# Performance work log

Hardware: AMD Instinct MI355X
Metric: run time of the kernel (lower is better)

Reference implementation:

```python
import jax, jax.numpy as jnp
import numpy as np

D_MODEL = 1024
N_HEADS = 16
D_K = D_MODEL // N_HEADS


def setup_inputs() -> dict:
    key = jax.random.key(0)
    ks = jax.random.split(key, 11)
    B, S = 2, 2048
    scale = 1.0 / np.sqrt(D_MODEL)
    return {
        "query": jax.random.normal(ks[0], (B, S, D_MODEL), jnp.float32),
        "key": jax.random.normal(ks[1], (B, S, D_MODEL), jnp.float32),
        "value": jax.random.normal(ks[2], (B, S, D_MODEL), jnp.float32),
        "w_q": jax.random.normal(ks[3], (D_MODEL, D_MODEL), jnp.float32) * scale,
        "b_q": jnp.zeros((D_MODEL,), jnp.float32),
        "w_k": jax.random.normal(ks[4], (D_MODEL, D_MODEL), jnp.float32) * scale,
        "b_k": jnp.zeros((D_MODEL,), jnp.float32),
        "w_v": jax.random.normal(ks[5], (D_MODEL, D_MODEL), jnp.float32) * scale,
        "b_v": jnp.zeros((D_MODEL,), jnp.float32),
        "w_o": jax.random.normal(ks[6], (D_MODEL, D_MODEL), jnp.float32) * scale,
        "b_o": jnp.zeros((D_MODEL,), jnp.float32),
    }


def reference(query, key, value, w_q, b_q, w_k, b_k, w_v, b_v, w_o, b_o):
    B, S, _ = query.shape
    # Linear projections (torch Linear: x @ W.T + b), split heads -> (B, H, S, Dk)
    def proj(x, w, b):
        y = jnp.einsum('bsd,ed->bse', x, w) + b
        return y.reshape(B, -1, N_HEADS, D_K).transpose(0, 2, 1, 3)
    q = proj(query, w_q, b_q)
    k = proj(key, w_k, b_k)
    v = proj(value, w_v, b_v)
    # Scaled dot-product attention (full O(S^2) scores, faithful to source)
    scores = jnp.einsum('bhqd,bhkd->bhqk', q, k) / np.sqrt(D_K)
    attn = jax.nn.softmax(scores, axis=-1)
    out = jnp.einsum('bhqk,bhkd->bhqd', attn, v)  # (B, H, S, Dk)
    out = out.transpose(0, 2, 1, 3).reshape(B, S, D_MODEL)
    out = jnp.einsum('bsd,ed->bse', out, w_o) + b_o
    return out
```

## Files before the change

kernel.cpp:

```cpp
#include <hip/hip_runtime.h>
#include <hip/hip_bf16.h>

#define DM 1024
#define NH 16
#define DKH 64
#define BB 2
#define SS 2048
#define MM (BB*SS)

typedef __bf16 v8bf __attribute__((ext_vector_type(8)));
typedef float  v4f  __attribute__((ext_vector_type(4)));
typedef float  v16f __attribute__((ext_vector_type(16)));

__device__ __forceinline__ unsigned short f2bf(float f) {
    union { float f; unsigned int u; } v; v.f = f;
    unsigned int u = v.u;
    unsigned int r = (u + 0x7fffu + ((u >> 16) & 1u)) >> 16;
    return (unsigned short)r;
}

__device__ __forceinline__ int cvtpk(float lo, float hi) {
    int r;
    asm("v_cvt_pk_bf16_f32 %0, %1, %2" : "=v"(r) : "v"(lo), "v"(hi));
    return r;
}

__device__ __forceinline__ void pl32swap(int& a, int& b) {
    asm("v_permlane32_swap_b32 %0, %1" : "+v"(a), "+v"(b));
}

__device__ __forceinline__ void gl16(const unsigned short* g, unsigned short* l) {
    auto gp = reinterpret_cast<const __attribute__((address_space(1))) unsigned int*>(
        reinterpret_cast<uintptr_t>(g));
    auto lp = reinterpret_cast<__attribute__((address_space(3))) unsigned int*>(
        reinterpret_cast<uintptr_t>(l));
    __builtin_amdgcn_global_load_lds(gp, lp, 16, 0, 0);
}

__global__ __launch_bounds__(256) void cvt_to_bf16(
    const float* __restrict__ xq, const float* __restrict__ xk, const float* __restrict__ xv,
    const float* __restrict__ wq, const float* __restrict__ wk, const float* __restrict__ wv,
    const float* __restrict__ wo, unsigned short* __restrict__ dst)
{
    const int y = blockIdx.y;
    const float* src;
    size_t n, off;
    if (y < 3) {
        src = (y == 0) ? xq : (y == 1) ? xk : xv;
        n = (size_t)MM * DM;
        off = (size_t)y * MM * DM;
    } else {
        src = (y == 3) ? wq : (y == 4) ? wk : (y == 5) ? wv : wo;
        n = (size_t)DM * DM;
        off = (size_t)3 * MM * DM + (size_t)(y - 3) * DM * DM;
    }
    unsigned short* d = dst + off;
    const size_t stride = (size_t)gridDim.x * blockDim.x;
    for (size_t i = (size_t)blockIdx.x * blockDim.x + threadIdx.x; i * 8 < n; i += stride) {
        float4 a = ((const float4*)src)[2 * i];
        float4 b = ((const float4*)src)[2 * i + 1];
        uint4 o;
        o.x = (unsigned)cvtpk(a.x, a.y);
        o.y = (unsigned)cvtpk(a.z, a.w);
        o.z = (unsigned)cvtpk(b.x, b.y);
        o.w = (unsigned)cvtpk(b.z, b.w);
        ((uint4*)d)[i] = o;
    }
}

__global__ __launch_bounds__(256) void proj_qkv_b(
    const unsigned short* __restrict__ xb, const unsigned short* __restrict__ wb,
    const float* __restrict__ bq, const float* __restrict__ bk, const float* __restrict__ bv,
    unsigned short* __restrict__ q_ws, unsigned short* __restrict__ k_ws,
    unsigned short* __restrict__ vt_ws)
{
    const int z = blockIdx.z;
    const unsigned short* X = xb + (size_t)z * MM * DM;
    const unsigned short* W = wb + (size_t)z * DM * DM;
    const float* bias = (z == 0) ? bq : (z == 1) ? bk : bv;

    __shared__ unsigned short lA[2][128 * 32];
    __shared__ unsigned short lB[2][128 * 32];

    const int t = threadIdx.x;
    const int lane = t & 63, w = t >> 6;
    const int wm = w >> 1, wn = w & 1;
    const int g = lane >> 4, lr = lane & 15;

    const int orig = blockIdx.y * 8 + blockIdx.x;
    const int swz = (orig & 7) * 32 + (orig >> 3);
    const int mbase = (swz >> 3) * 128;
    const int nbase = (swz & 7) * 128;

    const int srow = lane >> 2;
    const int scol = (lane & 3) * 8;

    v4f acc[4][4];
#pragma unroll
    for (int i = 0; i < 4; ++i)
#pragma unroll
        for (int j = 0; j < 4; ++j)
            acc[i][j] = (v4f){0.f, 0.f, 0.f, 0.f};

    auto stage = [&](int bi, int kb) {
        gl16(X + (size_t)(mbase + w * 16 + srow) * DM + kb + scol,      &lA[bi][w * 512]);
        gl16(X + (size_t)(mbase + 64 + w * 16 + srow) * DM + kb + scol, &lA[bi][(w + 4) * 512]);
        gl16(W + (size_t)(nbase + w * 16 + srow) * DM + kb + scol,      &lB[bi][w * 512]);
        gl16(W + (size_t)(nbase + 64 + w * 16 + srow) * DM + kb + scol, &lB[bi][(w + 4) * 512]);
    };

    stage(0, 0);
    __syncthreads();
    int buf = 0;
    for (int ki = 0; ki < 32; ++ki) {
        if (ki + 1 < 32) stage(buf ^ 1, (ki + 1) * 32);

        v8bf af[4], bf4[4];
#pragma unroll
        for (int mt = 0; mt < 4; ++mt)
            af[mt] = *(const v8bf*)(&lA[buf][(wm * 64 + mt * 16 + lr) * 32 + g * 8]);
#pragma unroll
        for (int nt = 0; nt < 4; ++nt)
            bf4[nt] = *(const v8bf*)(&lB[buf][(wn * 64 + nt * 16 + lr) * 32 + g * 8]);
#pragma unroll
        for (int mt = 0; mt < 4; ++mt)
#pragma unroll
            for (int nt = 0; nt < 4; ++nt)
                acc[mt][nt] = __builtin_amdgcn_mfma_f32_16x16x32_bf16(af[mt], bf4[nt], acc[mt][nt], 0, 0, 0);

        __syncthreads();
        buf ^= 1;
    }

    const float scale = (z == 0) ? 0.18033688011112042f : 1.0f;
#pragma unroll
    for (int nt = 0; nt < 4; ++nt) {
        int e = nbase + wn * 64 + nt * 16 + lr;
        float bval = bias[e];
        int h = e >> 6, dk = e & 63;
#pragma unroll
        for (int mt = 0; mt < 4; ++mt) {
#pragma unroll
            for (int r = 0; r < 4; ++r) {
                int m = mbase + wm * 64 + mt * 16 + g * 4 + r;
                float val = (acc[mt][nt][r] + bval) * scale;
                unsigned short o = f2bf(val);
                int b = m >> 11, s = m & 2047;
                if (z == 2) {
                    vt_ws[((size_t)(b * NH + h) * DKH + dk) * SS + s] = o;
                } else {
                    unsigned short* dst = (z == 0) ? q_ws : k_ws;
                    dst[((size_t)(b * NH + h) * SS + s) * DKH + dk] = o;
                }
            }
        }
    }
}

#define KB 64
#define LDP 72
#define BUFS 4608

__global__ __launch_bounds__(256) void attn_kernel(
    const unsigned short* __restrict__ q_ws, const unsigned short* __restrict__ k_ws,
    const unsigned short* __restrict__ vt_ws, unsigned short* __restrict__ o_ws)
{
    __shared__ unsigned short lsBuf[2 * 2 * BUFS];

    const int t = threadIdx.x, l = t & 63, w = t >> 6;
    const int h = l >> 5, ql = l & 31;
    const int id = blockIdx.x;
    const int swzb = (id & 7) * 64 + (id >> 3);
    const int bh = swzb >> 4, qb = swzb & 15;
    const int q0 = qb * 128 + w * 32;

    const unsigned short* Kbase = k_ws + (size_t)bh * SS * DKH;
    const unsigned short* Vbase = vt_ws + (size_t)bh * DKH * SS;

    v8bf qf[4];
#pragma unroll
    for (int c = 0; c < 4; ++c)
        qf[c] = *(const v8bf*)(q_ws + ((size_t)bh * SS + q0 + ql) * DKH + c * 16 + h * 8);

    v16f oT[2];
#pragma unroll
    for (int d = 0; d < 2; ++d)
#pragma unroll
        for (int r = 0; r < 16; ++r) oT[d][r] = 0.f;
    float l_lane = 0.f;
    const v16f z16 = {};

    const int r0 = t >> 3, c0 = (t & 7) * 8;
    uint4 kst0, kst1, vst0, vst1;

    kst0 = *(const uint4*)(Kbase + (size_t)(r0)      * DKH + c0);
    kst1 = *(const uint4*)(Kbase + (size_t)(r0 + 32) * DKH + c0);
    vst0 = *(const uint4*)(Vbase + (size_t)(r0)      * SS + c0);
    vst1 = *(const uint4*)(Vbase + (size_t)(r0 + 32) * SS + c0);
    {
        unsigned short* Kp = lsBuf;
        unsigned short* Vp = lsBuf + BUFS;
        *(uint4*)&Kp[r0 * LDP + c0] = kst0;
        *(uint4*)&Kp[(r0 + 32) * LDP + c0] = kst1;
        *(uint4*)&Vp[r0 * LDP + c0] = vst0;
        *(uint4*)&Vp[(r0 + 32) * LDP + c0] = vst1;
    }
    kst0 = *(const uint4*)(Kbase + (size_t)(KB + r0)      * DKH + c0);
    kst1 = *(const uint4*)(Kbase + (size_t)(KB + r0 + 32) * DKH + c0);
    vst0 = *(const uint4*)(Vbase + (size_t)(r0)      * SS + KB + c0);
    vst1 = *(const uint4*)(Vbase + (size_t)(r0 + 32) * SS + KB + c0);
    __syncthreads();

    const int NT = SS / KB;
    int p = 0;
    for (int tt = 0; tt < NT; ++tt) {
        unsigned short* Kp = lsBuf + p * (2 * BUFS);
        unsigned short* Vp = Kp + BUFS;
        if (tt + 1 < NT) {
            unsigned short* Kn = lsBuf + (p ^ 1) * (2 * BUFS);
            unsigned short* Vn = Kn + BUFS;
            *(uint4*)&Kn[r0 * LDP + c0] = kst0;
            *(uint4*)&Kn[(r0 + 32) * LDP + c0] = kst1;
            *(uint4*)&Vn[r0 * LDP + c0] = vst0;
            *(uint4*)&Vn[(r0 + 32) * LDP + c0] = vst1;
        }
        if (tt + 2 < NT) {
            int kt2 = (tt + 2) * KB;
            kst0 = *(const uint4*)(Kbase + (size_t)(kt2 + r0)      * DKH + c0);
            kst1 = *(const uint4*)(Kbase + (size_t)(kt2 + r0 + 32) * DKH + c0);
            vst0 = *(const uint4*)(Vbase + (size_t)(r0)      * SS + kt2 + c0);
            vst1 = *(const uint4*)(Vbase + (size_t)(r0 + 32) * SS + kt2 + c0);
        }

        v16f sT[2];
        __builtin_amdgcn_s_setprio(1);
#pragma unroll
        for (int kb = 0; kb < 2; ++kb) {
            v8bf kf = *(const v8bf*)&Kp[(kb * 32 + ql) * LDP + h * 8];
            sT[kb] = __builtin_amdgcn_mfma_f32_32x32x16_bf16(kf, qf[0], z16, 0, 0, 0);
        }
#pragma unroll
        for (int c = 1; c < 4; ++c)
#pragma unroll
            for (int kb = 0; kb < 2; ++kb) {
                v8bf kf = *(const v8bf*)&Kp[(kb * 32 + ql) * LDP + c * 16 + h * 8];
                sT[kb] = __builtin_amdgcn_mfma_f32_32x32x16_bf16(kf, qf[c], sT[kb], 0, 0, 0);
            }
        __builtin_amdgcn_s_setprio(0);

        float rs0 = 0.f, rs1 = 0.f, rs2 = 0.f, rs3 = 0.f;
#pragma unroll
        for (int kb = 0; kb < 2; ++kb)
#pragma unroll
            for (int r = 0; r < 16; r += 4) {
                float e0 = __builtin_amdgcn_exp2f(sT[kb][r + 0]);
                float e1 = __builtin_amdgcn_exp2f(sT[kb][r + 1]);
                float e2 = __builtin_amdgcn_exp2f(sT[kb][r + 2]);
                float e3 = __builtin_amdgcn_exp2f(sT[kb][r + 3]);
                sT[kb][r + 0] = e0; sT[kb][r + 1] = e1;
                sT[kb][r + 2] = e2; sT[kb][r + 3] = e3;
                rs0 += e0; rs1 += e1; rs2 += e2; rs3 += e3;
            }
        l_lane += (rs0 + rs1) + (rs2 + rs3);

        v8bf pfrag[4];
#pragma unroll
        for (int c = 0; c < 4; ++c) {
            const int cc = c & 1, kb = c >> 1;
            int A0 = cvtpk(sT[kb][8 * cc + 0], sT[kb][8 * cc + 1]);
            int A1 = cvtpk(sT[kb][8 * cc + 2], sT[kb][8 * cc + 3]);
            int B0 = cvtpk(sT[kb][8 * cc + 4], sT[kb][8 * cc + 5]);
            int B1 = cvtpk(sT[kb][8 * cc + 6], sT[kb][8 * cc + 7]);
            pl32swap(A0, B0);
            pl32swap(A1, B1);
            union { int i[4]; v8bf v; } u;
            u.i[0] = A0; u.i[1] = A1; u.i[2] = B0; u.i[3] = B1;
            pfrag[c] = u.v;
        }

        __builtin_amdgcn_s_setprio(1);
#pragma unroll
        for (int db = 0; db < 2; ++db)
#pragma unroll
            for (int c = 0; c < 4; ++c) {
                v8bf vf = *(const v8bf*)&Vp[(db * 32 + ql) * LDP + c * 16 + h * 8];
                oT[db] = __builtin_amdgcn_mfma_f32_32x32x16_bf16(vf, pfrag[c], oT[db], 0, 0, 0);
            }
        __builtin_amdgcn_s_setprio(0);

        __syncthreads();
        p ^= 1;
    }

    float l_run = l_lane + __shfl_xor(l_lane, 32);
    float inv = 1.0f / l_run;
    unsigned short* lO = lsBuf;
    const int row = w * 32 + ql;
#pragma unroll
    for (int db = 0; db < 2; ++db)
#pragma unroll
        for (int a = 0; a < 4; ++a) {
            int dbase = db * 32 + 8 * a + 4 * h;
            int pk0 = cvtpk(oT[db][4 * a + 0] * inv, oT[db][4 * a + 1] * inv);
            int pk1 = cvtpk(oT[db][4 * a + 2] * inv, oT[db][4 * a + 3] * inv);
            *(unsigned int*)&lO[row * LDP + dbase]     = pk0;
            *(unsigned int*)&lO[row * LDP + dbase + 2] = pk1;
        }
    __syncthreads();

    const int b = bh >> 4, hh = bh & 15;
#pragma unroll
    for (int i = 0; i < 4; ++i) {
        int idx = i * 256 + t;
        int orow = idx >> 3;
        int c8 = (idx & 7) * 8;
        int s = qb * 128 + orow;
        *(uint4*)(o_ws + ((size_t)b * SS + s) * DM + hh * DKH + c8) =
            *(const uint4*)&lO[orow * LDP + c8];
    }
}

__global__ __launch_bounds__(256) void proj_o_b(
    const unsigned short* __restrict__ A, const unsigned short* __restrict__ W,
    const float* __restrict__ bo, float* __restrict__ out)
{
    __shared__ unsigned short lA[2][128 * 32];
    __shared__ unsigned short lB[2][128 * 32];

    const int t = threadIdx.x;
    const int lane = t & 63, w = t >> 6;
    const int wm = w >> 1, wn = w & 1;
    const int g = lane >> 4, lr = lane & 15;

    const int orig = blockIdx.y * 8 + blockIdx.x;
    const int swz = (orig & 7) * 32 + (orig >> 3);
    const int mbase = (swz >> 3) * 128;
    const int nbase = (swz & 7) * 128;

    const int srow = lane >> 2;
    const int scol = (lane & 3) * 8;

    v4f acc[4][4];
#pragma unroll
    for (int i = 0; i < 4; ++i)
#pragma unroll
        for (int j = 0; j < 4; ++j)
            acc[i][j] = (v4f){0.f, 0.f, 0.f, 0.f};

    auto stage = [&](int bi, int kb) {
        gl16(A + (size_t)(mbase + w * 16 + srow) * DM + kb + scol,      &lA[bi][w * 512]);
        gl16(A + (size_t)(mbase + 64 + w * 16 + srow) * DM + kb + scol, &lA[bi][(w + 4) * 512]);
        gl16(W + (size_t)(nbase + w * 16 + srow) * DM + kb + scol,      &lB[bi][w * 512]);
        gl16(W + (size_t)(nbase + 64 + w * 16 + srow) * DM + kb + scol, &lB[bi][(w + 4) * 512]);
    };

    stage(0, 0);
    __syncthreads();
    int buf = 0;
    for (int ki = 0; ki < 32; ++ki) {
        if (ki + 1 < 32) stage(buf ^ 1, (ki + 1) * 32);

        v8bf af[4], bf4[4];
#pragma unroll
        for (int mt = 0; mt < 4; ++mt)
            af[mt] = *(const v8bf*)(&lA[buf][(wm * 64 + mt * 16 + lr) * 32 + g * 8]);
#pragma unroll
        for (int nt = 0; nt < 4; ++nt)
            bf4[nt] = *(const v8bf*)(&lB[buf][(wn * 64 + nt * 16 + lr) * 32 + g * 8]);
#pragma unroll
        for (int mt = 0; mt < 4; ++mt)
#pragma unroll
            for (int nt = 0; nt < 4; ++nt)
                acc[mt][nt] = __builtin_amdgcn_mfma_f32_16x16x32_bf16(af[mt], bf4[nt], acc[mt][nt], 0, 0, 0);

        __syncthreads();
        buf ^= 1;
    }

#pragma unroll
    for (int nt = 0; nt < 4; ++nt) {
        int e = nbase + wn * 64 + nt * 16 + lr;
        float bval = bo[e];
#pragma unroll
        for (int mt = 0; mt < 4; ++mt) {
#pragma unroll
            for (int r = 0; r < 4; ++r) {
                int m = mbase + wm * 64 + mt * 16 + g * 4 + r;
                out[(size_t)m * DM + e] = acc[mt][nt][r] + bval;
            }
        }
    }
}

extern "C" void kernel_launch(void* const* d_in, const int* in_sizes, int n_in,
                              void* d_out, int out_size, void* d_ws, size_t ws_size,
                              hipStream_t stream) {
    const float* q  = (const float*)d_in[0];
    const float* k  = (const float*)d_in[1];
    const float* v  = (const float*)d_in[2];
    const float* wq = (const float*)d_in[3];
    const float* bq = (const float*)d_in[4];
    const float* wk = (const float*)d_in[5];
    const float* bk = (const float*)d_in[6];
    const float* wv = (const float*)d_in[7];
    const float* bv = (const float*)d_in[8];
    const float* wo = (const float*)d_in[9];
    const float* bo = (const float*)d_in[10];
    float* out = (float*)d_out;

    unsigned short* ws    = (unsigned short*)d_ws;
    unsigned short* q_ws  = ws;
    unsigned short* k_ws  = q_ws + (size_t)MM * DM;
    unsigned short* vt_ws = k_ws + (size_t)MM * DM;
    unsigned short* xb    = vt_ws + (size_t)MM * DM;
    unsigned short* wb    = xb + (size_t)3 * MM * DM;
    unsigned short* o_ws  = xb;

    cvt_to_bf16<<<dim3(256, 7), 256, 0, stream>>>(q, k, v, wq, wk, wv, wo, xb);
    proj_qkv_b<<<dim3(8, 32, 3), 256, 0, stream>>>(xb, wb, bq, bk, bv, q_ws, k_ws, vt_ws);
    attn_kernel<<<dim3(512), 256, 0, stream>>>(q_ws, k_ws, vt_ws, o_ws);
    proj_o_b<<<dim3(8, 32), 256, 0, stream>>>(o_ws, wb + (size_t)3 * DM * DM, bo, out);
}
```

Baseline: 133.5 us.

## Split attention KV range across two wave groups and merge partial outputs

```diff
diff --git a/kernel.cpp b/kernel.cpp
--- a/kernel.cpp
+++ b/kernel.cpp
@@ -7,6 +7,7 @@
 #define BB 2
 #define SS 2048
 #define MM (BB*SS)
+#define HKB 1024
 
 typedef __bf16 v8bf __attribute__((ext_vector_type(8)));
 typedef float  v4f  __attribute__((ext_vector_type(4)));
@@ -87,10 +88,10 @@
     const int wm = w >> 1, wn = w & 1;
     const int g = lane >> 4, lr = lane & 15;
 
-    const int orig = blockIdx.y * 8 + blockIdx.x;
-    const int swz = (orig & 7) * 32 + (orig >> 3);
-    const int mbase = (swz >> 3) * 128;
-    const int nbase = (swz & 7) * 128;
+    const int hid = blockIdx.y * 8 + blockIdx.x;
+    const int xcd = hid & 7, slot = hid >> 3;
+    const int mbase = (xcd * 4 + (slot & 3)) * 128;
+    const int nbase = (slot >> 2) * 128;
 
     const int srow = lane >> 2;
     const int scol = (lane & 3) * 8;
@@ -159,23 +160,26 @@
 
 #define KB 64
 #define LDP 72
-#define BUFS 4608
-
-__global__ __launch_bounds__(256) void attn_kernel(
+#define TILE 4608
+
+__global__ __launch_bounds__(512, 4) void attn_kernel(
     const unsigned short* __restrict__ q_ws, const unsigned short* __restrict__ k_ws,
     const unsigned short* __restrict__ vt_ws, unsigned short* __restrict__ o_ws)
 {
-    __shared__ unsigned short lsBuf[2 * 2 * BUFS];
+    __shared__ __align__(16) unsigned short lsBuf[2 * 4 * TILE];
 
     const int t = threadIdx.x, l = t & 63, w = t >> 6;
     const int h = l >> 5, ql = l & 31;
-    const int id = blockIdx.x;
-    const int swzb = (id & 7) * 64 + (id >> 3);
-    const int bh = swzb >> 4, qb = swzb & 15;
-    const int q0 = qb * 128 + w * 32;
-
-    const unsigned short* Kbase = k_ws + (size_t)bh * SS * DKH;
-    const unsigned short* Vbase = vt_ws + (size_t)bh * DKH * SS;
+    const int qg = w >> 1, hf = w & 1;
+
+    const int hid = blockIdx.x;
+    const int slot = hid >> 3;
+    const int bh = (hid & 7) * 4 + (slot & 3);
+    const int qp = slot >> 2;
+    const int q0 = qp * 128 + qg * 32;
+
+    const unsigned short* Kb = k_ws + (size_t)bh * SS * DKH;
+    const unsigned short* Vb = vt_ws + (size_t)bh * DKH * SS;
 
     v8bf qf[4];
 #pragma unroll
@@ -190,46 +194,44 @@
     float l_lane = 0.f;
     const v16f z16 = {};
 
-    const int r0 = t >> 3, c0 = (t & 7) * 8;
-    uint4 kst0, kst1, vst0, vst1;
-
-    kst0 = *(const uint4*)(Kbase + (size_t)(r0)      * DKH + c0);
-    kst1 = *(const uint4*)(Kbase + (size_t)(r0 + 32) * DKH + c0);
-    vst0 = *(const uint4*)(Vbase + (size_t)(r0)      * SS + c0);
-    vst1 = *(const uint4*)(Vbase + (size_t)(r0 + 32) * SS + c0);
+    const int r0s = t >> 3, c0s = (t & 7) * 8;
+    uint4 k0r, k1r, v0r, v1r;
+
+    k0r = *(const uint4*)(Kb + (size_t)(r0s) * DKH + c0s);
+    v0r = *(const uint4*)(Vb + (size_t)r0s * SS + c0s);
+    k1r = *(const uint4*)(Kb + (size_t)(HKB + r0s) * DKH + c0s);
+    v1r = *(const uint4*)(Vb + (size_t)r0s * SS + HKB + c0s);
     {
-        unsigned short* Kp = lsBuf;
-        unsigned short* Vp = lsBuf + BUFS;
-        *(uint4*)&Kp[r0 * LDP + c0] = kst0;
-        *(uint4*)&Kp[(r0 + 32) * LDP + c0] = kst1;
-        *(uint4*)&Vp[r0 * LDP + c0] = vst0;
-        *(uint4*)&Vp[(r0 + 32) * LDP + c0] = vst1;
-    }
-    kst0 = *(const uint4*)(Kbase + (size_t)(KB + r0)      * DKH + c0);
-    kst1 = *(const uint4*)(Kbase + (size_t)(KB + r0 + 32) * DKH + c0);
-    vst0 = *(const uint4*)(Vbase + (size_t)(r0)      * SS + KB + c0);
-    vst1 = *(const uint4*)(Vbase + (size_t)(r0 + 32) * SS + KB + c0);
+        unsigned short* B0 = lsBuf;
+        *(uint4*)&B0[0 * TILE + r0s * LDP + c0s] = k0r;
+        *(uint4*)&B0[1 * TILE + r0s * LDP + c0s] = v0r;
+        *(uint4*)&B0[2 * TILE + r0s * LDP + c0s] = k1r;
+        *(uint4*)&B0[3 * TILE + r0s * LDP + c0s] = v1r;
+    }
+    k0r = *(const uint4*)(Kb + (size_t)(KB + r0s) * DKH + c0s);
+    v0r = *(const uint4*)(Vb + (size_t)r0s * SS + KB + c0s);
+    k1r = *(const uint4*)(Kb + (size_t)(HKB + KB + r0s) * DKH + c0s);
+    v1r = *(const uint4*)(Vb + (size_t)r0s * SS + HKB + KB + c0s);
     __syncthreads();
 
-    const int NT = SS / KB;
+    const int NT = 16;
     int p = 0;
     for (int tt = 0; tt < NT; ++tt) {
-        unsigned short* Kp = lsBuf + p * (2 * BUFS);
-        unsigned short* Vp = Kp + BUFS;
+        unsigned short* Kp = lsBuf + p * (4 * TILE) + hf * (2 * TILE);
+        unsigned short* Vp = Kp + TILE;
         if (tt + 1 < NT) {
-            unsigned short* Kn = lsBuf + (p ^ 1) * (2 * BUFS);
-            unsigned short* Vn = Kn + BUFS;
-            *(uint4*)&Kn[r0 * LDP + c0] = kst0;
-            *(uint4*)&Kn[(r0 + 32) * LDP + c0] = kst1;
-            *(uint4*)&Vn[r0 * LDP + c0] = vst0;
-            *(uint4*)&Vn[(r0 + 32) * LDP + c0] = vst1;
+            unsigned short* Bn = lsBuf + (p ^ 1) * (4 * TILE);
+            *(uint4*)&Bn[0 * TILE + r0s * LDP + c0s] = k0r;
+            *(uint4*)&Bn[1 * TILE + r0s * LDP + c0s] = v0r;
+            *(uint4*)&Bn[2 * TILE + r0s * LDP + c0s] = k1r;
+            *(uint4*)&Bn[3 * TILE + r0s * LDP + c0s] = v1r;
         }
         if (tt + 2 < NT) {
             int kt2 = (tt + 2) * KB;
-            kst0 = *(const uint4*)(Kbase + (size_t)(kt2 + r0)      * DKH + c0);
-            kst1 = *(const uint4*)(Kbase + (size_t)(kt2 + r0 + 32) * DKH + c0);
-            vst0 = *(const uint4*)(Vbase + (size_t)(r0)      * SS + kt2 + c0);
-            vst1 = *(const uint4*)(Vbase + (size_t)(r0 + 32) * SS + kt2 + c0);
+            k0r = *(const uint4*)(Kb + (size_t)(kt2 + r0s) * DKH + c0s);
+            v0r = *(const uint4*)(Vb + (size_t)r0s * SS + kt2 + c0s);
+            k1r = *(const uint4*)(Kb + (size_t)(HKB + kt2 + r0s) * DKH + c0s);
+            v1r = *(const uint4*)(Vb + (size_t)r0s * SS + HKB + kt2 + c0s);
         }
 
         v16f sT[2];
@@ -292,32 +294,38 @@
         p ^= 1;
     }
 
-    float l_run = l_lane + __shfl_xor(l_lane, 32);
-    float inv = 1.0f / l_run;
-    unsigned short* lO = lsBuf;
-    const int row = w * 32 + ql;
+    float lsum = l_lane + __shfl_xor(l_lane, 32);
+    float* lsf = (float*)lsBuf;
+    const int row = qg * 32 + ql;
 #pragma unroll
     for (int db = 0; db < 2; ++db)
 #pragma unroll
-        for (int a = 0; a < 4; ++a) {
-            int dbase = db * 32 + 8 * a + 4 * h;
-            int pk0 = cvtpk(oT[db][4 * a + 0] * inv, oT[db][4 * a + 1] * inv);
-            int pk1 = cvtpk(oT[db][4 * a + 2] * inv, oT[db][4 * a + 3] * inv);
-            *(unsigned int*)&lO[row * LDP + dbase]     = pk0;
-            *(unsigned int*)&lO[row * LDP + dbase + 2] = pk1;
-        }
+        for (int r = 0; r < 16; ++r) {
+            int d = db * 32 + (r & 3) + 8 * (r >> 2) + 4 * h;
+            lsf[(hf * 128 + row) * 65 + d] = oT[db][r];
+        }
+    if (h == 0) lsf[(hf * 128 + row) * 65 + 64] = lsum;
     __syncthreads();
 
+    const int orow = t >> 2;
+    const int ck = t & 3;
+    const float* e0 = lsf + orow * 65;
+    const float* e1 = lsf + (128 + orow) * 65;
+    const float linv = 1.0f / (e0[64] + e1[64]);
     const int b = bh >> 4, hh = bh & 15;
-#pragma unroll
-    for (int i = 0; i < 4; ++i) {
-        int idx = i * 256 + t;
-        int orow = idx >> 3;
-        int c8 = (idx & 7) * 8;
-        int s = qb * 128 + orow;
-        *(uint4*)(o_ws + ((size_t)b * SS + s) * DM + hh * DKH + c8) =
-            *(const uint4*)&lO[orow * LDP + c8];
-    }
+    const int d0 = ck * 16;
+    unsigned short* op = o_ws + ((size_t)b * SS + qp * 128 + orow) * DM + hh * DKH + d0;
+    uint4 o0, o1;
+    o0.x = (unsigned)cvtpk((e0[d0+0]+e1[d0+0])*linv,  (e0[d0+1]+e1[d0+1])*linv);
+    o0.y = (unsigned)cvtpk((e0[d0+2]+e1[d0+2])*linv,  (e0[d0+3]+e1[d0+3])*linv);
+    o0.z = (unsigned)cvtpk((e0[d0+4]+e1[d0+4])*linv,  (e0[d0+5]+e1[d0+5])*linv);
+    o0.w = (unsigned)cvtpk((e0[d0+6]+e1[d0+6])*linv,  (e0[d0+7]+e1[d0+7])*linv);
+    o1.x = (unsigned)cvtpk((e0[d0+8]+e1[d0+8])*linv,  (e0[d0+9]+e1[d0+9])*linv);
+    o1.y = (unsigned)cvtpk((e0[d0+10]+e1[d0+10])*linv,(e0[d0+11]+e1[d0+11])*linv);
+    o1.z = (unsigned)cvtpk((e0[d0+12]+e1[d0+12])*linv,(e0[d0+13]+e1[d0+13])*linv);
+    o1.w = (unsigned)cvtpk((e0[d0+14]+e1[d0+14])*linv,(e0[d0+15]+e1[d0+15])*linv);
+    *(uint4*)op = o0;
+    *(uint4*)(op + 8) = o1;
 }
 
 __global__ __launch_bounds__(256) void proj_o_b(
@@ -332,10 +340,10 @@
     const int wm = w >> 1, wn = w & 1;
     const int g = lane >> 4, lr = lane & 15;
 
-    const int orig = blockIdx.y * 8 + blockIdx.x;
-    const int swz = (orig & 7) * 32 + (orig >> 3);
-    const int mbase = (swz >> 3) * 128;
-    const int nbase = (swz & 7) * 128;
+    const int hid = blockIdx.y * 8 + blockIdx.x;
+    const int xcd = hid & 7, slot = hid >> 3;
+    const int mbase = (xcd * 4 + (slot & 3)) * 128;
+    const int nbase = (slot >> 2) * 128;
 
     const int srow = lane >> 2;
     const int scol = (lane & 3) * 8;
@@ -418,6 +426,6 @@
 
     cvt_to_bf16<<<dim3(256, 7), 256, 0, stream>>>(q, k, v, wq, wk, wv, wo, xb);
     proj_qkv_b<<<dim3(8, 32, 3), 256, 0, stream>>>(xb, wb, bq, bk, bv, q_ws, k_ws, vt_ws);
-    attn_kernel<<<dim3(512), 256, 0, stream>>>(q_ws, k_ws, vt_ws, o_ws);
+    attn_kernel<<<dim3(512), 512, 0, stream>>>(q_ws, k_ws, vt_ws, o_ws);
     proj_o_b<<<dim3(8, 32), 256, 0, stream>>>(o_ws, wb + (size_t)3 * DM * DM, bo, out);
 }
```

Result: faster. 128.8 us (-3.5%).
